# Performance work log

Measured on AMD Instinct MI355X. Metric: run time of the kernel, lower is better.

## Reference

```python
import jax, jax.numpy as jnp
import numpy as np

B, R, H = 64, 32, 1024  # batch, num_rounds, lstm_hidden_size
IN = 2 * H              # GatedTrans in_dim
EPS = 1e-12             # F.normalize eps


def _gated(x, Wy, by, Wg, bg):
    # GatedTrans: tanh branch * leaky_relu branch (slope 0.01, torch default)
    return jnp.tanh(x @ Wy + by) * jax.nn.leaky_relu(x @ Wg + bg, 0.01)


def setup_inputs() -> dict:
    key = jax.random.key(0)
    ks = jax.random.split(key, 12)
    s_in = 1.0 / np.sqrt(IN)
    s_h = 1.0 / np.sqrt(H)
    return {
        "hist": jax.random.normal(ks[0], (B, R, IN), jnp.float32),
        "ques": jax.random.normal(ks[1], (B, R, IN), jnp.float32),
        "W_hy": jax.random.normal(ks[2], (IN, H), jnp.float32) * s_in,
        "b_hy": jnp.zeros((H,), jnp.float32),
        "W_hg": jax.random.normal(ks[3], (IN, H), jnp.float32) * s_in,
        "b_hg": jnp.zeros((H,), jnp.float32),
        "W_qy": jax.random.normal(ks[4], (IN, H), jnp.float32) * s_in,
        "b_qy": jnp.zeros((H,), jnp.float32),
        "W_qg": jax.random.normal(ks[5], (IN, H), jnp.float32) * s_in,
        "b_qg": jnp.zeros((H,), jnp.float32),
        "W_att": jax.random.normal(ks[6], (H,), jnp.float32) * s_h,
        "b_att": jnp.zeros((), jnp.float32),
    }


def reference(hist, ques, W_hy, b_hy, W_hg, b_hg, W_qy, b_qy, W_qg, b_qg, W_att, b_att):
    hist_embed = _gated(hist, W_hy, b_hy, W_hg, b_hg)   # [B, R, H]
    ques_embed = _gated(ques, W_qy, b_qy, W_qg, b_qg)   # [B, R, H]
    # broadcast outer product over rounds: [B, Rq, Rh, H]
    att_embed = ques_embed[:, :, None, :] * hist_embed[:, None, :, :]
    norm = jnp.sqrt(jnp.sum(att_embed * att_embed, axis=-1, keepdims=True))
    att_embed = att_embed / jnp.maximum(norm, EPS)       # F.normalize(p=2)
    scores = att_embed @ W_att + b_att                   # [B, Rq, Rh]
    att = jax.nn.softmax(scores, axis=-1)
    tril = jnp.tril(jnp.ones((R, R), jnp.float32))       # causal round mask
    att_masked = att * tril
    att_masked = att_masked / jnp.sum(att_masked, axis=-1, keepdims=True)
    # weighted sum over hist rounds: [B, Rq, 2H]
    feat = jnp.einsum("bqh,bhd->bqd", att_masked, hist)
    return feat
```

## Files before the change

kernel.cpp:

```cpp
#include <hip/hip_runtime.h>
#include <cstdint>

#define IN_DIM 2048
#define H_DIM  1024
#define BROWS  2048
#define BATCH  64
#define ROUNDS 32

typedef __bf16 bf16x8 __attribute__((ext_vector_type(8)));
typedef float  f32x4  __attribute__((ext_vector_type(4)));
typedef unsigned short u16;
typedef u16 u16x8 __attribute__((ext_vector_type(8)));

__device__ __forceinline__ u16 f2bf(float f) {
    unsigned int u = __float_as_uint(f);
    u += 0x7FFFu + ((u >> 16) & 1u);
    return (u16)(u >> 16);
}

__device__ __forceinline__ void async_ld16(const void* g, void* l) {
    __builtin_amdgcn_global_load_lds(
        (__attribute__((address_space(1))) void*)(uintptr_t)g,
        (__attribute__((address_space(3))) void*)(unsigned int)(uintptr_t)l,
        16, 0, 0);
}

#define BAR()    asm volatile("s_barrier" ::: "memory")
#define LGKM0()  asm volatile("s_waitcnt lgkmcnt(0)" ::: "memory")
#define VMCNT4() asm volatile("s_waitcnt vmcnt(4)" ::: "memory")
#define VMCNT0() asm volatile("s_waitcnt vmcnt(0)" ::: "memory")

__global__ __launch_bounds__(256) void prep(
    const float* __restrict__ hist, const float* __restrict__ ques,
    u16* __restrict__ xh, u16* __restrict__ xq,
    const float* __restrict__ why, const float* __restrict__ whg,
    const float* __restrict__ wqy, const float* __restrict__ wqg,
    u16* __restrict__ oh, u16* __restrict__ oq)
{
    int idx = blockIdx.x;
    if (idx < 4096) {
        int i = idx * 256 + threadIdx.x;
        const float4* h4 = (const float4*)hist;
        const float4* q4 = (const float4*)ques;
        float4 a = h4[i], b = q4[i];
        ushort4 oa, ob;
        oa.x = f2bf(a.x); oa.y = f2bf(a.y); oa.z = f2bf(a.z); oa.w = f2bf(a.w);
        ob.x = f2bf(b.x); ob.y = f2bf(b.y); ob.z = f2bf(b.z); ob.w = f2bf(b.w);
        ((ushort4*)xh)[i] = oa;
        ((ushort4*)xq)[i] = ob;
        return;
    }
    int zz = idx - 4096;
    int z  = zz >> 9;
    int rem = zz & 511;
    int bk = rem >> 5;
    int bn = rem & 31;
    const float* Y = z == 0 ? why : wqy;
    const float* G = z == 0 ? whg : wqg;
    u16* O = z == 0 ? oh : oq;
    int k0 = bk << 7, c0 = bn << 5, n0 = bn << 6;

    __shared__ float t[2][128][33];
    int tid = threadIdx.x;
    int row = tid >> 3, cg = (tid & 7) << 2;
    #pragma unroll
    for (int p = 0; p < 4; p++) {
        int k = row + 32 * p;
        float4 vy = *(const float4*)&Y[(size_t)(k0 + k) * H_DIM + c0 + cg];
        float4 vg = *(const float4*)&G[(size_t)(k0 + k) * H_DIM + c0 + cg];
        t[0][k][cg + 0] = vy.x; t[0][k][cg + 1] = vy.y;
        t[0][k][cg + 2] = vy.z; t[0][k][cg + 3] = vy.w;
        t[1][k][cg + 0] = vg.x; t[1][k][cg + 1] = vg.y;
        t[1][k][cg + 2] = vg.z; t[1][k][cg + 3] = vg.w;
    }
    __syncthreads();
    int j4 = tid >> 4, kg = tid & 15;
    #pragma unroll
    for (int p = 0; p < 4; p++) {
        int j = j4 + 16 * p;
        int mat = (j >> 4) & 1;
        int lc = ((j >> 5) << 4) | (j & 15);
        u16x8 pk;
        #pragma unroll
        for (int e = 0; e < 8; e++)
            pk[e] = f2bf(t[mat][kg * 8 + e][lc]);
        *(u16x8*)&O[(size_t)(n0 + j) * IN_DIM + k0 + kg * 8] = pk;
    }
}

__global__ __launch_bounds__(256, 4) void gemm_act(
    const u16* __restrict__ xh, const u16* __restrict__ xq,
    const u16* __restrict__ wth, const u16* __restrict__ wtq,
    const float* __restrict__ bhy, const float* __restrict__ bhg,
    const float* __restrict__ bqy, const float* __restrict__ bqg,
    u16* __restrict__ eh, u16* __restrict__ eq)
{
    int L = blockIdx.x;
    int cluster = L & 7;
    int slot = L >> 3;
    int z = cluster >> 2;
    int y = (cluster & 1) * 8 + (slot >> 3);
    int x = ((cluster >> 1) & 1) * 8 + (slot & 7);
    int m0 = y * 128, n0 = x * 128;

    const u16* A  = z == 0 ? xh : xq;
    const u16* Bt = z == 0 ? wth : wtq;
    const float* by = z == 0 ? bhy : bqy;
    const float* bg = z == 0 ? bhg : bqg;
    u16* E = z == 0 ? eh : eq;

    __shared__ __align__(16) u16 As[2][128 * 32];
    __shared__ __align__(16) u16 Bs[2][128 * 32];

    int tid = threadIdx.x;
    int wave = tid >> 6, lane = tid & 63;
    int lane15 = lane & 15, quad = lane >> 4;
    int wm = (wave >> 1) * 64, wn = (wave & 1) * 64;

    f32x4 acc[4][4];
    #pragma unroll
    for (int i = 0; i < 4; i++)
        #pragma unroll
        for (int j = 0; j < 4; j++) acc[i][j] = (f32x4){0.f, 0.f, 0.f, 0.f};

    int aoff[2], boff[2], cb[2];
    #pragma unroll
    for (int r2 = 0; r2 < 2; r2++) {
        int cs = r2 * 256 + tid;
        int row = cs >> 2, p = cs & 3;
        int l = p ^ ((row >> 1) & 3);
        aoff[r2] = (m0 + row) * IN_DIM + l * 8;
        boff[r2] = (n0 + row) * IN_DIM + l * 8;
        cb[r2]   = r2 * 256 + wave * 64;
    }

    #define STAGE(buf, kt)                                                                    \
        _Pragma("unroll")                                                                     \
        for (int r2 = 0; r2 < 2; r2++) {                                                      \
            async_ld16(A  + (size_t)aoff[r2] + (kt), &As[buf][cb[r2] * 8]);                   \
            async_ld16(Bt + (size_t)boff[r2] + (kt), &Bs[buf][cb[r2] * 8]);                   \
        }

    bf16x8 af[4], bfv[4];

    #define DSREAD(buf)                                                                       \
        _Pragma("unroll")                                                                     \
        for (int i = 0; i < 4; i++) {                                                         \
            int row = wm + i * 16 + lane15;                                                   \
            int p = quad ^ ((row >> 1) & 3);                                                  \
            af[i] = *(const bf16x8*)&As[buf][row * 32 + p * 8];                               \
            int rowb = wn + i * 16 + lane15;                                                  \
            int pb = quad ^ ((rowb >> 1) & 3);                                                \
            bfv[i] = *(const bf16x8*)&Bs[buf][rowb * 32 + pb * 8];                            \
        }

    #define MFMA16()                                                                          \
        __builtin_amdgcn_s_setprio(1);                                                        \
        _Pragma("unroll")                                                                     \
        for (int i = 0; i < 4; i++)                                                           \
            _Pragma("unroll")                                                                 \
            for (int j = 0; j < 4; j++)                                                       \
                acc[i][j] = __builtin_amdgcn_mfma_f32_16x16x32_bf16(                          \
                    af[i], bfv[j], acc[i][j], 0, 0, 0);                                       \
        __builtin_amdgcn_s_setprio(0);

    #define TILE(t, buf)                                                                      \
        DSREAD(buf)                                                                           \
        LGKM0(); BAR();                                                                       \
        if ((t) + 2 < 64) { STAGE(buf, ((t) + 2) * 32) }                                      \
        MFMA16()                                                                              \
        if ((t) + 2 < 64) { VMCNT4(); } else { VMCNT0(); }                                    \
        if ((t) < 63) { BAR(); }

    STAGE(0, 0)
    STAGE(1, 32)
    VMCNT4(); BAR();

    #pragma unroll 1
    for (int t2 = 0; t2 < 64; t2 += 2) {
        TILE(t2, 0)
        TILE(t2 + 1, 1)
    }
    #undef STAGE
    #undef DSREAD
    #undef MFMA16
    #undef TILE

    int n0w = n0 + wn;
    #pragma unroll
    for (int jp = 0; jp < 2; jp++) {
        int hc = (n0w >> 1) + jp * 16 + lane15;
        float vy = by[hc], vg = bg[hc];
        #pragma unroll
        for (int i = 0; i < 4; i++) {
            #pragma unroll
            for (int r = 0; r < 4; r++) {
                int row = m0 + wm + i * 16 + quad * 4 + r;
                float y2 = tanhf(acc[i][2 * jp][r] + vy);
                float g = acc[i][2 * jp + 1][r] + vg;
                E[(size_t)row * H_DIM + hc] = f2bf(y2 * (g > 0.f ? g : 0.01f * g));
            }
        }
    }
}

__global__ __launch_bounds__(256) void score_feat(
    const u16* __restrict__ eh, const u16* __restrict__ eq,
    const float* __restrict__ hist, const float* __restrict__ watt,
    const float* __restrict__ batt, float* __restrict__ out)
{
    int idx = blockIdx.x;
    int b = idx & 63, q = idx >> 6;
    int tid = threadIdx.x, wave = tid >> 6, lane = tid & 63;
    __shared__ float sw[32], swn[32];

    const u16* qe = eq + (size_t)(b * ROUNDS + q) * H_DIM;
    float uw[16], u2[16];
    #pragma unroll
    for (int c = 0; c < 2; c++) {
        uint4 pk = ((const uint4*)qe)[lane + 64 * c];
        float4 w0 = ((const float4*)watt)[(lane + 64 * c) * 2];
        float4 w1 = ((const float4*)watt)[(lane + 64 * c) * 2 + 1];
        unsigned int ws[4] = {pk.x, pk.y, pk.z, pk.w};
        float wf[8] = {w0.x, w0.y, w0.z, w0.w, w1.x, w1.y, w1.z, w1.w};
        #pragma unroll
        for (int e = 0; e < 4; e++) {
            float lo = __uint_as_float(ws[e] << 16);
            float hi = __uint_as_float(ws[e] & 0xFFFF0000u);
            uw[c * 8 + 2 * e]     = lo * wf[2 * e];
            u2[c * 8 + 2 * e]     = lo * lo;
            uw[c * 8 + 2 * e + 1] = hi * wf[2 * e + 1];
            u2[c * 8 + 2 * e + 1] = hi * hi;
        }
    }
    for (int h = wave; h <= q; h += 4) {
        const u16* he = eh + (size_t)(b * ROUNDS + h) * H_DIM;
        float num = 0.f, nrm = 0.f;
        #pragma unroll
        for (int c = 0; c < 2; c++) {
            uint4 pk = ((const uint4*)he)[lane + 64 * c];
            unsigned int vs[4] = {pk.x, pk.y, pk.z, pk.w};
            #pragma unroll
            for (int e = 0; e < 4; e++) {
                float lo = __uint_as_float(vs[e] << 16);
                float hi = __uint_as_float(vs[e] & 0xFFFF0000u);
                num += uw[c * 8 + 2 * e] * lo + uw[c * 8 + 2 * e + 1] * hi;
                nrm += u2[c * 8 + 2 * e] * lo * lo + u2[c * 8 + 2 * e + 1] * hi * hi;
            }
        }
        #pragma unroll
        for (int off = 32; off > 0; off >>= 1) {
            num += __shfl_down(num, off);
            nrm += __shfl_down(nrm, off);
        }
        if (lane == 0)
            sw[h] = num / fmaxf(sqrtf(nrm), 1e-12f) + batt[0];
    }
    __syncthreads();
    if (tid < 64) {
        int h = lane & 31;
        bool v = (h <= q);
        float s = v ? sw[h] : -1e30f;
        float mx = s;
        #pragma unroll
        for (int off = 16; off > 0; off >>= 1)
            mx = fmaxf(mx, __shfl_xor(mx, off));
        float e = v ? expf(s - mx) : 0.f;
        float zs = e;
        #pragma unroll
        for (int off = 16; off > 0; off >>= 1)
            zs += __shfl_xor(zs, off);
        if (v && lane < 32) swn[h] = e / zs;
    }
    __syncthreads();
    const float4* hb = (const float4*)(hist + (size_t)b * ROUNDS * IN_DIM);
    float4* ob = (float4*)(out + (size_t)(b * ROUNDS + q) * IN_DIM);
    #pragma unroll
    for (int d0 = 0; d0 < 2; d0++) {
        int d = tid + d0 * 256;
        float4 a = {0.f, 0.f, 0.f, 0.f};
        for (int h = 0; h <= q; h++) {
            float w = swn[h];
            float4 x = hb[h * 512 + d];
            a.x += w * x.x; a.y += w * x.y; a.z += w * x.z; a.w += w * x.w;
        }
        ob[d] = a;
    }
}

extern "C" void kernel_launch(void* const* d_in, const int* in_sizes, int n_in,
                              void* d_out, int out_size, void* d_ws, size_t ws_size,
                              hipStream_t stream) {
    const float* hist = (const float*)d_in[0];
    const float* ques = (const float*)d_in[1];
    const float* Why  = (const float*)d_in[2];
    const float* bhy  = (const float*)d_in[3];
    const float* Whg  = (const float*)d_in[4];
    const float* bhg  = (const float*)d_in[5];
    const float* Wqy  = (const float*)d_in[6];
    const float* bqy  = (const float*)d_in[7];
    const float* Wqg  = (const float*)d_in[8];
    const float* bqg  = (const float*)d_in[9];
    const float* watt = (const float*)d_in[10];
    const float* batt = (const float*)d_in[11];
    float* out = (float*)d_out;

    char* w = (char*)d_ws;
    u16* Xh  = (u16*)w;
    u16* Xq  = Xh  + (size_t)BROWS * IN_DIM;
    u16* WtH = Xq  + (size_t)BROWS * IN_DIM;
    u16* WtQ = WtH + (size_t)IN_DIM * IN_DIM;
    u16* Eh  = WtQ + (size_t)IN_DIM * IN_DIM;
    u16* Eq  = Eh  + (size_t)BROWS * H_DIM;

    prep<<<5120, 256, 0, stream>>>(hist, ques, Xh, Xq, Why, Whg, Wqy, Wqg, WtH, WtQ);
    gemm_act<<<512, 256, 0, stream>>>(Xh, Xq, WtH, WtQ, bhy, bhg, bqy, bqg, Eh, Eq);
    score_feat<<<2048, 256, 0, stream>>>(Eh, Eq, hist, watt, batt, out);
}
```

Before: 184.9 us.

## Split GEMM K dimension across two wave groups with shared-memory reduction

The GEMM block grows to 512 threads, split into two groups of four waves. Each group handles half of the K range with its own double-buffered LDS tiles, and the partial accumulators are summed through shared memory before the gated activation epilogue. The goal is more waves per block to hide latency in a tall-K GEMM with few blocks. In exchange it drops the hand-tuned vmcnt/barrier pipeline in favour of plain __syncthreads, adds a reduction step, and raises LDS use to 64KB per block, which may limit occupancy.

Result: slower. 218.7 us (+18.3%).

```diff
diff --git a/kernel.cpp b/kernel.cpp
--- a/kernel.cpp
+++ b/kernel.cpp
@@ -24,11 +24,6 @@
         (__attribute__((address_space(3))) void*)(unsigned int)(uintptr_t)l,
         16, 0, 0);
 }
-
-#define BAR()    asm volatile("s_barrier" ::: "memory")
-#define LGKM0()  asm volatile("s_waitcnt lgkmcnt(0)" ::: "memory")
-#define VMCNT4() asm volatile("s_waitcnt vmcnt(4)" ::: "memory")
-#define VMCNT0() asm volatile("s_waitcnt vmcnt(0)" ::: "memory")
 
 __global__ __launch_bounds__(256) void prep(
     const float* __restrict__ hist, const float* __restrict__ ques,
@@ -88,7 +83,7 @@
     }
 }
 
-__global__ __launch_bounds__(256, 4) void gemm_act(
+__global__ __launch_bounds__(512, 4) void gemm_act(
     const u16* __restrict__ xh, const u16* __restrict__ xq,
     const u16* __restrict__ wth, const u16* __restrict__ wtq,
     const float* __restrict__ bhy, const float* __restrict__ bhg,
@@ -109,13 +104,16 @@
     const float* bg = z == 0 ? bhg : bqg;
     u16* E = z == 0 ? eh : eq;
 
-    __shared__ __align__(16) u16 As[2][128 * 32];
-    __shared__ __align__(16) u16 Bs[2][128 * 32];
+    __shared__ __align__(16) u16 smem[32768];
 
     int tid = threadIdx.x;
     int wave = tid >> 6, lane = tid & 63;
+    int g = wave >> 2;
+    int qd = wave & 3;
     int lane15 = lane & 15, quad = lane >> 4;
-    int wm = (wave >> 1) * 64, wn = (wave & 1) * 64;
+    int wm = (qd >> 1) * 64, wn = (qd & 1) * 64;
+    int tidg = tid & 255;
+    int kbase = g << 10;
 
     f32x4 acc[4][4];
     #pragma unroll
@@ -126,32 +124,40 @@
     int aoff[2], boff[2], cb[2];
     #pragma unroll
     for (int r2 = 0; r2 < 2; r2++) {
-        int cs = r2 * 256 + tid;
+        int cs = r2 * 256 + tidg;
         int row = cs >> 2, p = cs & 3;
         int l = p ^ ((row >> 1) & 3);
-        aoff[r2] = (m0 + row) * IN_DIM + l * 8;
-        boff[r2] = (n0 + row) * IN_DIM + l * 8;
-        cb[r2]   = r2 * 256 + wave * 64;
-    }
-
-    #define STAGE(buf, kt)                                                                    \
-        _Pragma("unroll")                                                                     \
-        for (int r2 = 0; r2 < 2; r2++) {                                                      \
-            async_ld16(A  + (size_t)aoff[r2] + (kt), &As[buf][cb[r2] * 8]);                   \
-            async_ld16(Bt + (size_t)boff[r2] + (kt), &Bs[buf][cb[r2] * 8]);                   \
+        aoff[r2] = (m0 + row) * IN_DIM + kbase + l * 8;
+        boff[r2] = (n0 + row) * IN_DIM + kbase + l * 8;
+        cb[r2]   = (r2 * 256 + qd * 64) * 8;
+    }
+
+    #define STAGE(buf, ktrel)                                                                 \
+        {                                                                                     \
+            u16* sA = smem + ((g * 2 + (buf)) << 12);                                         \
+            u16* sB = smem + 16384 + ((g * 2 + (buf)) << 12);                                 \
+            _Pragma("unroll")                                                                 \
+            for (int r2 = 0; r2 < 2; r2++) {                                                  \
+                async_ld16(A  + (size_t)(aoff[r2] + (ktrel)), sA + cb[r2]);                   \
+                async_ld16(Bt + (size_t)(boff[r2] + (ktrel)), sB + cb[r2]);                   \
+            }                                                                                 \
         }
 
     bf16x8 af[4], bfv[4];
 
     #define DSREAD(buf)                                                                       \
-        _Pragma("unroll")                                                                     \
-        for (int i = 0; i < 4; i++) {                                                         \
-            int row = wm + i * 16 + lane15;                                                   \
-            int p = quad ^ ((row >> 1) & 3);                                                  \
-            af[i] = *(const bf16x8*)&As[buf][row * 32 + p * 8];                               \
-            int rowb = wn + i * 16 + lane15;                                                  \
-            int pb = quad ^ ((rowb >> 1) & 3);                                                \
-            bfv[i] = *(const bf16x8*)&Bs[buf][rowb * 32 + pb * 8];                            \
+        {                                                                                     \
+            u16* sA = smem + ((g * 2 + (buf)) << 12);                                         \
+            u16* sB = smem + 16384 + ((g * 2 + (buf)) << 12);                                 \
+            _Pragma("unroll")                                                                 \
+            for (int i = 0; i < 4; i++) {                                                     \
+                int row = wm + i * 16 + lane15;                                               \
+                int p = quad ^ ((row >> 1) & 3);                                              \
+                af[i] = *(const bf16x8*)&sA[row * 32 + p * 8];                                \
+                int rowb = wn + i * 16 + lane15;                                              \
+                int pb = quad ^ ((rowb >> 1) & 3);                                            \
+                bfv[i] = *(const bf16x8*)&sB[rowb * 32 + pb * 8];                             \
+            }                                                                                 \
         }
 
     #define MFMA16()                                                                          \
@@ -164,41 +170,56 @@
                     af[i], bfv[j], acc[i][j], 0, 0, 0);                                       \
         __builtin_amdgcn_s_setprio(0);
 
-    #define TILE(t, buf)                                                                      \
-        DSREAD(buf)                                                                           \
-        LGKM0(); BAR();                                                                       \
-        if ((t) + 2 < 64) { STAGE(buf, ((t) + 2) * 32) }                                      \
-        MFMA16()                                                                              \
-        if ((t) + 2 < 64) { VMCNT4(); } else { VMCNT0(); }                                    \
-        if ((t) < 63) { BAR(); }
-
     STAGE(0, 0)
-    STAGE(1, 32)
-    VMCNT4(); BAR();
+    __syncthreads();
 
     #pragma unroll 1
-    for (int t2 = 0; t2 < 64; t2 += 2) {
-        TILE(t2, 0)
-        TILE(t2 + 1, 1)
+    for (int t2 = 0; t2 < 32; t2 += 2) {
+        if (t2 + 1 < 32) STAGE(1, (t2 + 1) * 32)
+        DSREAD(0)
+        MFMA16()
+        __syncthreads();
+        if (t2 + 2 < 32) STAGE(0, (t2 + 2) * 32)
+        DSREAD(1)
+        MFMA16()
+        __syncthreads();
     }
     #undef STAGE
     #undef DSREAD
     #undef MFMA16
-    #undef TILE
-
-    int n0w = n0 + wn;
-    #pragma unroll
-    for (int jp = 0; jp < 2; jp++) {
-        int hc = (n0w >> 1) + jp * 16 + lane15;
-        float vy = by[hc], vg = bg[hc];
-        #pragma unroll
-        for (int i = 0; i < 4; i++) {
+
+    float* xch = (float*)smem;
+    if (g == 1) {
+        #pragma unroll
+        for (int i = 0; i < 4; i++)
             #pragma unroll
-            for (int r = 0; r < 4; r++) {
-                int row = m0 + wm + i * 16 + quad * 4 + r;
-                float y2 = tanhf(acc[i][2 * jp][r] + vy);
-                float g = acc[i][2 * jp + 1][r] + vg;
-                E[(size_t)row * H_DIM + hc] = f2bf(y2 * (g > 0.f ? g : 0.01f * g));
+            for (int j = 0; j < 4; j++)
+                *(f32x4*)&xch[qd * 4096 + (i * 4 + j) * 256 + lane * 4] = acc[i][j];
+    }
+    __syncthreads();
+    if (g == 0) {
+        #pragma unroll
+        for (int i = 0; i < 4; i++)
+            #pragma unroll
+            for (int j = 0; j < 4; j++) {
+                f32x4 o = *(const f32x4*)&xch[qd * 4096 + (i * 4 + j) * 256 + lane * 4];
+                acc[i][j].x += o.x; acc[i][j].y += o.y;
+                acc[i][j].z += o.z; acc[i][j].w += o.w;
+            }
+        int n0w = n0 + wn;
+        #pragma unroll
+        for (int jp = 0; jp < 2; jp++) {
+            int hc = (n0w >> 1) + jp * 16 + lane15;
+            float vy = by[hc], vg = bg[hc];
+            #pragma unroll
+            for (int i = 0; i < 4; i++) {
+                #pragma unroll
+                for (int r = 0; r < 4; r++) {
+                    int row = m0 + wm + i * 16 + quad * 4 + r;
+                    float y2 = tanhf(acc[i][2 * jp][r] + vy);
+                    float gg = acc[i][2 * jp + 1][r] + vg;
+                    E[(size_t)row * H_DIM + hc] = f2bf(y2 * (gg > 0.f ? gg : 0.01f * gg));
+                }
             }
         }
     }
@@ -314,6 +335,6 @@
     u16* Eq  = Eh  + (size_t)BROWS * H_DIM;
 
     prep<<<5120, 256, 0, stream>>>(hist, ques, Xh, Xq, Why, Whg, Wqy, Wqg, WtH, WtQ);
-    gemm_act<<<512, 256, 0, stream>>>(Xh, Xq, WtH, WtQ, bhy, bhg, bqy, bqg, Eh, Eq);
+    gemm_act<<<512, 512, 0, stream>>>(Xh, Xq, WtH, WtQ, bhy, bhg, bqy, bqg, Eh, Eq);
     score_feat<<<2048, 256, 0, stream>>>(Eh, Eq, hist, watt, batt, out);
 }
```

## Enlarge GEMM tile to 256x128 with 8 waves and 4-stage async pipeline

Applied to the files above, without the earlier changes.

Restructures the gated GEMM so each 512-thread workgroup computes a 256x128 output tile, which halves the workgroup count and raises reuse of the B tile. Staging moves to a 4-buffer ring with prefetch depth 3, and the LDS layout uses a new row-pair XOR swizzle. The explicit LDS-read wait before the barrier is dropped, and each iteration keeps a single barrier. This aims to cut global traffic and hide load latency, at the cost of one workgroup per CU (launch bounds 512,1) and fewer workgroups, 256, to spread across the device.

After: 181.7 us. About the same (-1.7%).

```diff
diff --git a/kernel.cpp b/kernel.cpp
--- a/kernel.cpp
+++ b/kernel.cpp
@@ -26,8 +26,8 @@
 }
 
 #define BAR()    asm volatile("s_barrier" ::: "memory")
-#define LGKM0()  asm volatile("s_waitcnt lgkmcnt(0)" ::: "memory")
-#define VMCNT4() asm volatile("s_waitcnt vmcnt(4)" ::: "memory")
+#define VMCNT6() asm volatile("s_waitcnt vmcnt(6)" ::: "memory")
+#define VMCNT3() asm volatile("s_waitcnt vmcnt(3)" ::: "memory")
 #define VMCNT0() asm volatile("s_waitcnt vmcnt(0)" ::: "memory")
 
 __global__ __launch_bounds__(256) void prep(
@@ -88,7 +88,7 @@
     }
 }
 
-__global__ __launch_bounds__(256, 4) void gemm_act(
+__global__ __launch_bounds__(512, 1) void gemm_act(
     const u16* __restrict__ xh, const u16* __restrict__ xq,
     const u16* __restrict__ wth, const u16* __restrict__ wtq,
     const float* __restrict__ bhy, const float* __restrict__ bhg,
@@ -99,9 +99,9 @@
     int cluster = L & 7;
     int slot = L >> 3;
     int z = cluster >> 2;
-    int y = (cluster & 1) * 8 + (slot >> 3);
+    int y = (cluster & 1) * 4 + (slot >> 3);
     int x = ((cluster >> 1) & 1) * 8 + (slot & 7);
-    int m0 = y * 128, n0 = x * 128;
+    int m0 = y * 256, n0 = x * 128;
 
     const u16* A  = z == 0 ? xh : xq;
     const u16* Bt = z == 0 ? wth : wtq;
@@ -109,13 +109,13 @@
     const float* bg = z == 0 ? bhg : bqg;
     u16* E = z == 0 ? eh : eq;
 
-    __shared__ __align__(16) u16 As[2][128 * 32];
-    __shared__ __align__(16) u16 Bs[2][128 * 32];
+    __shared__ __align__(16) u16 smem[49152];
 
     int tid = threadIdx.x;
     int wave = tid >> 6, lane = tid & 63;
     int lane15 = lane & 15, quad = lane >> 4;
-    int wm = (wave >> 1) * 64, wn = (wave & 1) * 64;
+    int wm = (wave & 3) * 64;
+    int wn = (wave >> 2) * 64;
 
     f32x4 acc[4][4];
     #pragma unroll
@@ -123,35 +123,48 @@
         #pragma unroll
         for (int j = 0; j < 4; j++) acc[i][j] = (f32x4){0.f, 0.f, 0.f, 0.f};
 
-    int aoff[2], boff[2], cb[2];
+    int aoff[2], acb[2], boff, bcb;
     #pragma unroll
     for (int r2 = 0; r2 < 2; r2++) {
-        int cs = r2 * 256 + tid;
-        int row = cs >> 2, p = cs & 3;
-        int l = p ^ ((row >> 1) & 3);
-        aoff[r2] = (m0 + row) * IN_DIM + l * 8;
-        boff[r2] = (n0 + row) * IN_DIM + l * 8;
-        cb[r2]   = r2 * 256 + wave * 64;
+        int cs = r2 * 512 + tid;
+        int row2 = cs >> 3, p8 = cs & 7;
+        int l8 = p8 ^ (row2 & 7);
+        aoff[r2] = (m0 + row2 * 2 + (l8 >> 2)) * IN_DIM + (l8 & 3) * 8;
+        acb[r2]  = (r2 * 512 + wave * 64) * 8;
+    }
+    {
+        int row2 = tid >> 3, p8 = tid & 7;
+        int l8 = p8 ^ (row2 & 7);
+        boff = (n0 + row2 * 2 + (l8 >> 2)) * IN_DIM + (l8 & 3) * 8;
+        bcb  = (wave * 64) * 8;
     }
 
     #define STAGE(buf, kt)                                                                    \
-        _Pragma("unroll")                                                                     \
-        for (int r2 = 0; r2 < 2; r2++) {                                                      \
-            async_ld16(A  + (size_t)aoff[r2] + (kt), &As[buf][cb[r2] * 8]);                   \
-            async_ld16(Bt + (size_t)boff[r2] + (kt), &Bs[buf][cb[r2] * 8]);                   \
+        {                                                                                     \
+            u16* sA = smem + (buf) * 12288;                                                   \
+            u16* sB = sA + 8192;                                                              \
+            async_ld16(A  + (size_t)(aoff[0] + (kt)), sA + acb[0]);                           \
+            async_ld16(A  + (size_t)(aoff[1] + (kt)), sA + acb[1]);                           \
+            async_ld16(Bt + (size_t)(boff    + (kt)), sB + bcb);                              \
         }
 
     bf16x8 af[4], bfv[4];
 
     #define DSREAD(buf)                                                                       \
-        _Pragma("unroll")                                                                     \
-        for (int i = 0; i < 4; i++) {                                                         \
-            int row = wm + i * 16 + lane15;                                                   \
-            int p = quad ^ ((row >> 1) & 3);                                                  \
-            af[i] = *(const bf16x8*)&As[buf][row * 32 + p * 8];                               \
-            int rowb = wn + i * 16 + lane15;                                                  \
-            int pb = quad ^ ((rowb >> 1) & 3);                                                \
-            bfv[i] = *(const bf16x8*)&Bs[buf][rowb * 32 + pb * 8];                            \
+        {                                                                                     \
+            const u16* sA = smem + (buf) * 12288;                                             \
+            const u16* sB = sA + 8192;                                                        \
+            _Pragma("unroll")                                                                 \
+            for (int i = 0; i < 4; i++) {                                                     \
+                int row = wm + i * 16 + lane15;                                               \
+                int r2w = row >> 1;                                                           \
+                int p8 = (((row & 1) << 2) | quad) ^ (r2w & 7);                               \
+                af[i] = *(const bf16x8*)&sA[r2w * 64 + p8 * 8];                               \
+                int rowb = wn + i * 16 + lane15;                                              \
+                int r2b = rowb >> 1;                                                          \
+                int pb8 = (((rowb & 1) << 2) | quad) ^ (r2b & 7);                             \
+                bfv[i] = *(const bf16x8*)&sB[r2b * 64 + pb8 * 8];                             \
+            }                                                                                 \
         }
 
     #define MFMA16()                                                                          \
@@ -164,27 +177,25 @@
                     af[i], bfv[j], acc[i][j], 0, 0, 0);                                       \
         __builtin_amdgcn_s_setprio(0);
 
-    #define TILE(t, buf)                                                                      \
-        DSREAD(buf)                                                                           \
-        LGKM0(); BAR();                                                                       \
-        if ((t) + 2 < 64) { STAGE(buf, ((t) + 2) * 32) }                                      \
-        MFMA16()                                                                              \
-        if ((t) + 2 < 64) { VMCNT4(); } else { VMCNT0(); }                                    \
-        if ((t) < 63) { BAR(); }
-
     STAGE(0, 0)
     STAGE(1, 32)
-    VMCNT4(); BAR();
+    STAGE(2, 64)
+    VMCNT6(); BAR();
 
     #pragma unroll 1
-    for (int t2 = 0; t2 < 64; t2 += 2) {
-        TILE(t2, 0)
-        TILE(t2 + 1, 1)
+    for (int t = 0; t < 64; ++t) {
+        int buf = t & 3;
+        DSREAD(buf)
+        if (t <= 60) STAGE((t + 3) & 3, (t + 3) * 32)
+        MFMA16()
+        if (t <= 60)      { VMCNT6(); }
+        else if (t == 61) { VMCNT3(); }
+        else if (t == 62) { VMCNT0(); }
+        if (t < 63) BAR();
     }
     #undef STAGE
     #undef DSREAD
     #undef MFMA16
-    #undef TILE
 
     int n0w = n0 + wn;
     #pragma unroll
@@ -314,6 +325,6 @@
     u16* Eq  = Eh  + (size_t)BROWS * H_DIM;
 
     prep<<<5120, 256, 0, stream>>>(hist, ques, Xh, Xq, Why, Whg, Wqy, Wqg, WtH, WtQ);
-    gemm_act<<<512, 256, 0, stream>>>(Xh, Xq, WtH, WtQ, bhy, bhg, bqy, bqg, Eh, Eq);
+    gemm_act<<<256, 512, 0, stream>>>(Xh, Xq, WtH, WtQ, bhy, bhg, bqy, bqg, Eh, Eq);
     score_feat<<<2048, 256, 0, stream>>>(Eh, Eq, hist, watt, batt, out);
 }
```
